# Performance work log

Measured on AMD Instinct MI355X. Metric: run time of the kernel, lower is better.

The kernel has to match this reference:

```python
import jax, jax.numpy as jnp
import numpy as np

K_MASK = -2.3819763e+38
NUM_HEADS = 16
NUM_KV_HEADS = 8
FEATURES = 2048
HEAD_DIM = 128
WINDOW = 1024
SOFT_CAP = 50.0
B, T = 2, 2048


def apply_rope(inputs, positions, head_dim, max_wavelength=10000):
    # inputs: [B, T, N, H], positions: [B, T]
    fraction = 2 * jnp.arange(0, head_dim // 2) / head_dim
    timescale = max_wavelength ** fraction
    sinusoid_inp = positions[..., None] / timescale[None, None, :]  # [B,T,H/2]
    sinusoid_inp = sinusoid_inp[..., None, :]  # [B,T,1,H/2]
    sin = jnp.sin(sinusoid_inp)
    cos = jnp.cos(sinusoid_inp)
    first_half, second_half = jnp.split(inputs, 2, axis=-1)
    first_part = first_half * cos - second_half * sin
    second_part = second_half * cos + first_half * sin
    return jnp.concatenate([first_part, second_part], axis=-1).astype(inputs.dtype)


def setup_inputs() -> dict:
    key = jax.random.key(0)
    k1, k2, k3, k4 = jax.random.split(key, 4)
    std = 0.02
    x = jax.random.normal(k1, (B, T, FEATURES), dtype=jnp.float32)
    segment_pos = jnp.broadcast_to(jnp.arange(T, dtype=jnp.int32), (B, T))
    # causal prefill mask [B, T, T]
    attn_mask = jnp.broadcast_to(jnp.tril(jnp.ones((T, T), dtype=bool)), (B, T, T))
    wq = jax.random.normal(k2, (NUM_HEADS, FEATURES, HEAD_DIM), dtype=jnp.float32) * std
    wkv = jax.random.normal(k3, (2, NUM_KV_HEADS, FEATURES, HEAD_DIM), dtype=jnp.float32) * std
    wo = jax.random.normal(k4, (NUM_HEADS, HEAD_DIM, FEATURES), dtype=jnp.float32) * std
    return {"x": x, "segment_pos": segment_pos, "attn_mask": attn_mask,
            "wq": wq, "wkv": wkv, "wo": wo}


def reference(x, segment_pos, attn_mask, wq, wkv, wo):
    # Projections (GQA path: num_kv_heads != num_heads)
    q = jnp.einsum('BTD,NDH->BTNH', x, wq)              # [B,T,N,H]
    k = jnp.einsum('BSD,KDH->BSKH', x, wkv[0])          # [B,S,K,H]
    v = jnp.einsum('BSD,KDH->BSKH', x, wkv[1])          # [B,S,K,H]

    q = apply_rope(q, segment_pos, HEAD_DIM)
    q = q * HEAD_DIM ** (-0.5)
    k = apply_rope(k, segment_pos, HEAD_DIM)

    b, t, n, h = q.shape
    g = n // NUM_KV_HEADS
    qg = q.reshape(b, t, NUM_KV_HEADS, g, h)
    logits = jnp.einsum('BTKGH,BSKH->BTKGS', qg, k)
    s = logits.shape[-1]
    logits = logits.reshape(b, t, n, s)

    # soft cap
    logits = jnp.tanh(logits / SOFT_CAP) * SOFT_CAP

    # sliding-window mask combined with attn_mask
    cache_positions = jnp.arange(s)[None, None, :]
    sp = segment_pos[:, :, None]
    sliding_mask = (cache_positions >= sp - WINDOW + 1) & (cache_positions <= sp + WINDOW - 1)
    mask = sliding_mask & attn_mask  # [B,T,S]

    padded_logits = jnp.where(mask[:, :, None, :], logits, K_MASK)
    probs = jax.nn.softmax(padded_logits, axis=-1).astype(k.dtype)

    pg = probs.reshape(b, t, NUM_KV_HEADS, g, s)
    encoded = jnp.einsum('BTKGS,BSKH->BTKGH', pg, v).reshape(b, t, n, h)
    attn_output = jnp.einsum('BTNH,NHD->BTD', encoded, wo)
    return attn_output
```

## Files before the change

### kernel.cpp

```cpp
#include <hip/hip_runtime.h>

typedef unsigned short u16;
typedef unsigned int u32;
typedef __attribute__((ext_vector_type(8))) short bfx8;
typedef __attribute__((ext_vector_type(4))) float fx4;

static __device__ __forceinline__ float b2f(u16 u) {
    union { float f; u32 i; } c; c.i = ((u32)u) << 16; return c.f;
}
static __device__ __forceinline__ u16 f2b(float f) {
    union { float f; u32 i; } c; c.f = f;
    u32 r = c.i + 0x7FFFu + ((c.i >> 16) & 1u);
    return (u16)(r >> 16);
}
typedef const __attribute__((address_space(1))) unsigned int* gas1;
typedef __attribute__((address_space(3))) unsigned int* las3;
static __device__ __forceinline__ void gll16(const void* g, void* l) {
    __builtin_amdgcn_global_load_lds((gas1)g, (las3)l, 16, 0, 0);
}

__global__ __launch_bounds__(256) void k_convert_x(const float* __restrict__ x, u16* __restrict__ xb) {
    size_t i = ((size_t)blockIdx.x * 256 + threadIdx.x) * 8;
    float4 a = *(const float4*)(x + i);
    float4 b = *(const float4*)(x + i + 4);
    union { u16 e[8]; uint4 v; } o;
    o.e[0] = f2b(a.x); o.e[1] = f2b(a.y); o.e[2] = f2b(a.z); o.e[3] = f2b(a.w);
    o.e[4] = f2b(b.x); o.e[5] = f2b(b.y); o.e[6] = f2b(b.z); o.e[7] = f2b(b.w);
    *(uint4*)(xb + i) = o.v;
}

__global__ __launch_bounds__(256) void k_pack_w1(const float* __restrict__ wq, const float* __restrict__ wkv,
                                                 u16* __restrict__ wb1) {
    __shared__ float t[128 * 33];
    int ci = blockIdx.x;
    int k0 = blockIdx.y << 5;
    int c0 = ci << 7;
    const float* src;
    if (ci < 16)      src = wq  + (size_t)ci * 2048 * 128;
    else if (ci < 24) src = wkv + (size_t)(ci - 16) * 2048 * 128;
    else              src = wkv + (size_t)(8 + ci - 24) * 2048 * 128;
    int tid = threadIdx.x;
#pragma unroll
    for (int i = 0; i < 16; i++) {
        int idx = i * 256 + tid;
        int kk = idx >> 7, cc = idx & 127;
        t[cc * 33 + kk] = src[(size_t)(k0 + kk) * 128 + cc];
    }
    __syncthreads();
#pragma unroll
    for (int i = 0; i < 16; i++) {
        int idx = i * 256 + tid;
        int cc = idx >> 5, kk = idx & 31;
        wb1[(size_t)(c0 + cc) * 2048 + k0 + kk] = f2b(t[cc * 33 + kk]);
    }
}

__global__ __launch_bounds__(256) void k_pack_w2(const float* __restrict__ wo, u16* __restrict__ wb2) {
    __shared__ float t[128 * 33];
    int c0 = blockIdx.x << 7;
    int k0 = blockIdx.y << 5;
    int tid = threadIdx.x;
#pragma unroll
    for (int i = 0; i < 16; i++) {
        int idx = i * 256 + tid;
        int kk = idx >> 7, cc = idx & 127;
        t[cc * 33 + kk] = wo[(size_t)(k0 + kk) * 2048 + c0 + cc];
    }
    __syncthreads();
#pragma unroll
    for (int i = 0; i < 16; i++) {
        int idx = i * 256 + tid;
        int cc = idx >> 5, kk = idx & 31;
        wb2[(size_t)(c0 + cc) * 2048 + k0 + kk] = f2b(t[cc * 33 + kk]);
    }
}

template <int BM, int OUT_BF16>
__global__ __launch_bounds__(512, 2) void k_gemm256(const u16* __restrict__ A, const u16* __restrict__ Bt,
                                                    void* __restrict__ C, int M, int N, int K) {
    constexpr int MF = BM / 32;
    constexpr int NA = BM / 16;
    constexpr int FR = NA + 16;
    constexpr int LPW = FR / 8;
    __shared__ u16 lds[4 * FR * 512];

    int tid = threadIdx.x, wave = tid >> 6, lane = tid & 63;
    int quad = lane >> 4, l16 = lane & 15;
    int wm = wave >> 2, wn = wave & 3;

    int nwg = gridDim.x * gridDim.y;
    int bid = blockIdx.y * gridDim.x + blockIdx.x;
    int swz = (bid & 7) * (nwg >> 3) + (bid >> 3);
    int bx = swz % gridDim.x, by = swz / gridDim.x;
    int r0 = by * BM, c0 = bx << 8;

    fx4 zero = {0.f, 0.f, 0.f, 0.f};
    fx4 acc[MF][4];
#pragma unroll
    for (int m = 0; m < MF; m++)
#pragma unroll
        for (int n = 0; n < 4; n++) acc[m][n] = zero;

    const u16* gsrc[LPW];
#pragma unroll
    for (int j = 0; j < LPW; j++) {
        int fw = wave * LPW + j;
        gsrc[j] = (fw < NA ? A + (size_t)(r0 + fw * 16 + l16) * K
                           : Bt + (size_t)(c0 + (fw - NA) * 16 + l16) * K) + quad * 8;
    }
    u16* ldst = lds + wave * (LPW * 512);

    int NT = K >> 5;
#pragma unroll
    for (int p = 0; p < 3; p++)
#pragma unroll
        for (int j = 0; j < LPW; j++) gll16(gsrc[j] + p * 32, ldst + p * (FR * 512) + j * 512);

    asm volatile("s_waitcnt vmcnt(%0)" : : "n"(2 * LPW) : "memory");
    __builtin_amdgcn_s_barrier();

    bfx8 cbf[4], caf[4];
#pragma unroll
    for (int n = 0; n < 4; n++) cbf[n] = *(const bfx8*)(lds + (NA + wn * 4 + n) * 512 + lane * 8);
#pragma unroll
    for (int m = 0; m < 4; m++) caf[m] = *(const bfx8*)(lds + (wm * MF + m) * 512 + lane * 8);

    for (int t = 0; t < NT; ++t) {
        const u16* Fb = lds + (t & 3) * (FR * 512);
        bfx8 nbf[4], naf[4], af1[4];
        bool has_next = (t + 1 < NT);
        if (has_next) {
            if (t + 2 < NT) asm volatile("s_waitcnt vmcnt(%0)" : : "n"(LPW) : "memory");
            else            asm volatile("s_waitcnt vmcnt(0)" : : : "memory");
            __builtin_amdgcn_s_barrier();
            if (t + 3 < NT) {
                u16* dst = lds + ((t + 3) & 3) * (FR * 512) + wave * (LPW * 512);
#pragma unroll
                for (int j = 0; j < LPW; j++) gll16(gsrc[j] + (size_t)(t + 3) * 32, dst + j * 512);
            }
        }
        if constexpr (MF == 8) {
#pragma unroll
            for (int m = 0; m < 4; m++) af1[m] = *(const bfx8*)(Fb + (wm * MF + 4 + m) * 512 + lane * 8);
        }
        if (has_next) {
            const u16* Fn = lds + ((t + 1) & 3) * (FR * 512);
#pragma unroll
            for (int n = 0; n < 4; n++) nbf[n] = *(const bfx8*)(Fn + (NA + wn * 4 + n) * 512 + lane * 8);
#pragma unroll
            for (int m = 0; m < 4; m++) naf[m] = *(const bfx8*)(Fn + (wm * MF + m) * 512 + lane * 8);
        }
        __builtin_amdgcn_s_setprio(1);
#pragma unroll
        for (int m = 0; m < 4; m++)
#pragma unroll
            for (int n = 0; n < 4; n++)
                acc[m][n] = __builtin_amdgcn_mfma_f32_16x16x32_bf16(caf[m], cbf[n], acc[m][n], 0, 0, 0);
        __builtin_amdgcn_s_setprio(0);
        if constexpr (MF == 8) {
            __builtin_amdgcn_s_setprio(1);
#pragma unroll
            for (int m = 0; m < 4; m++)
#pragma unroll
                for (int n = 0; n < 4; n++)
                    acc[4 + m][n] = __builtin_amdgcn_mfma_f32_16x16x32_bf16(af1[m], cbf[n], acc[4 + m][n], 0, 0, 0);
            __builtin_amdgcn_s_setprio(0);
        }
        if (has_next) {
#pragma unroll
            for (int n = 0; n < 4; n++) cbf[n] = nbf[n];
#pragma unroll
            for (int m = 0; m < 4; m++) caf[m] = naf[m];
        }
    }
#pragma unroll
    for (int m = 0; m < MF; m++)
#pragma unroll
        for (int n = 0; n < 4; n++) {
            int col = c0 + wn * 64 + n * 16 + l16;
#pragma unroll
            for (int r = 0; r < 4; r++) {
                int row = r0 + wm * (BM / 2) + m * 16 + quad * 4 + r;
                float v = acc[m][n][r];
                if (OUT_BF16) ((u16*)C)[(size_t)row * N + col] = f2b(v);
                else          ((float*)C)[(size_t)row * N + col] = v;
            }
        }
}

__global__ __launch_bounds__(256) void k_rope(const u16* __restrict__ qkv, u16* __restrict__ Qb,
                                              u16* __restrict__ Kb, u16* __restrict__ Vb) {
    __shared__ float sc[128];
    int bt = blockIdx.x;
    int b = bt >> 11, t = bt & 2047;
    const u16* row = qkv + (size_t)bt * 4096;
    int tid = threadIdx.x;
    float tf = (float)t;
    const float RS = 0.08838834764831845f;
    const float LT = 0.20762050593046f;
    if (tid < 64) {
        float ang = tf * exp2f(-LT * (float)tid);
        float s, c; sincosf(ang, &s, &c);
        sc[tid] = s; sc[tid + 64] = c;
    }
    __syncthreads();
#pragma unroll
    for (int i = 0; i < 4; i++) {
        int idx = tid + i * 256;
        int n = idx >> 6, hp = idx & 63;
        float x1 = b2f(row[n * 128 + hp]);
        float x2 = b2f(row[n * 128 + hp + 64]);
        float s = sc[hp], c = sc[hp + 64];
        size_t o = ((size_t)(b * 16 + n) * 2048 + t) * 128 + hp;
        Qb[o]      = f2b((x1 * c - x2 * s) * RS);
        Qb[o + 64] = f2b((x2 * c + x1 * s) * RS);
    }
#pragma unroll
    for (int i = 0; i < 2; i++) {
        int idx = tid + i * 256;
        int kh = idx >> 6, hp = idx & 63;
        float x1 = b2f(row[2048 + kh * 128 + hp]);
        float x2 = b2f(row[2048 + kh * 128 + hp + 64]);
        float s = sc[hp], c = sc[hp + 64];
        size_t o = ((size_t)(b * 8 + kh) * 2048 + t) * 128 + hp;
        Kb[o]      = f2b(x1 * c - x2 * s);
        Kb[o + 64] = f2b(x2 * c + x1 * s);
    }
#pragma unroll
    for (int i = 0; i < 4; i++) {
        int idx = tid + i * 256;
        int kh = idx >> 7, h = idx & 127;
        Vb[((size_t)(b * 8 + kh) * 2048 + t) * 128 + h] = row[3072 + idx];
    }
}

__global__ __launch_bounds__(256) void k_transpose_v(const u16* __restrict__ Vb, u16* __restrict__ Vt) {
    __shared__ u16 t[128 * 136];
    int bk = blockIdx.y;
    int t0 = blockIdx.x << 7;
    const u16* src = Vb + ((size_t)bk * 2048 + t0) * 128;
    u16* dst = Vt + (size_t)bk * 128 * 2048 + t0;
    int tid = threadIdx.x;
#pragma unroll
    for (int it = 0; it < 8; it++) {
        int ch = tid + it * 256;
        int tt = ch >> 4, c8 = (ch & 15) << 3;
        *(uint4*)(t + tt * 136 + c8) = *(const uint4*)(src + (size_t)tt * 128 + c8);
    }
    __syncthreads();
#pragma unroll
    for (int it = 0; it < 8; it++) {
        int ch = tid + it * 256;
        int h = ch >> 4, s8 = (ch & 15) << 3;
        union { uint4 v; u16 e[8]; } vv;
#pragma unroll
        for (int j = 0; j < 8; j++) vv.e[j] = t[(s8 + j) * 136 + h];
        *(uint4*)(dst + (size_t)h * 2048 + s8) = vv.v;
    }
}

__global__ __launch_bounds__(512, 4) void k_attn(const u16* __restrict__ Qb, const u16* __restrict__ Kb,
                                                 const u16* __restrict__ Vt, u16* __restrict__ enc) {
    __shared__ u16 Ks[2][16 * 512];
    __shared__ u16 Vs[2][16 * 512];
    __shared__ u16 Pl[8 * 1024];
    int t0 = blockIdx.x << 6;
    int kh = blockIdx.y, b = blockIdx.z;
    int tid = threadIdx.x, wave = tid >> 6, lane = tid & 63;
    int quad = lane >> 4, l16 = lane & 15;
    int n = (kh << 1) + (wave >> 2);
    int tw = t0 + ((wave & 3) << 4);
    const u16* Qp = Qb + (size_t)(b * 16 + n) * 2048 * 128;
    const u16* Kp = Kb + (size_t)(b * 8 + kh) * 2048 * 128;
    const u16* Vp = Vt + (size_t)(b * 8 + kh) * 128 * 2048;

    bfx8 aq[4];
#pragma unroll
    for (int kb = 0; kb < 4; kb++)
        aq[kb] = *(const bfx8*)(Qp + (size_t)(tw + l16) * 128 + kb * 32 + quad * 8);

    const u16* kgp[2]; const u16* vgp[2];
#pragma unroll
    for (int q = 0; q < 2; q++) {
        int f = wave * 2 + q;
        kgp[q] = Kp + (size_t)((f >> 2) * 16 + l16) * 128 + (f & 3) * 32 + quad * 8;
        vgp[q] = Vp + (size_t)((f >> 1) * 16 + l16) * 2048 + (f & 1) * 32 + quad * 8;
    }
    u16* Pw = Pl + wave * 1024;

    fx4 zero = {0.f, 0.f, 0.f, 0.f};
    fx4 o_acc[8];
#pragma unroll
    for (int hb = 0; hb < 8; hb++) o_acc[hb] = zero;
    float lsum[4] = {0.f, 0.f, 0.f, 0.f};

    const float C1 = 0.057707801635559f;
    const float C2 = 144.269504088896f;

    int s_lo = t0 - 1023; if (s_lo < 0) s_lo = 0;
    int ts0 = s_lo >> 6, ts1 = t0 >> 6;

#pragma unroll
    for (int q = 0; q < 2; q++) {
        int f = wave * 2 + q;
        gll16(kgp[q] + (size_t)(ts0 << 6) * 128, Ks[0] + f * 512);
        gll16(vgp[q] + (ts0 << 6), Vs[0] + f * 512);
    }

    for (int ts = ts0; ts <= ts1; ts++) {
        int cur = (ts - ts0) & 1;
        int s0 = ts << 6;
        __builtin_amdgcn_s_barrier();
        if (ts < ts1) {
            int s1 = (ts + 1) << 6;
#pragma unroll
            for (int q = 0; q < 2; q++) {
                int f = wave * 2 + q;
                gll16(kgp[q] + (size_t)s1 * 128, Ks[cur ^ 1] + f * 512);
                gll16(vgp[q] + s1, Vs[cur ^ 1] + f * 512);
            }
            asm volatile("s_waitcnt vmcnt(4)" : : : "memory");
        } else {
            asm volatile("s_waitcnt vmcnt(0)" : : : "memory");
        }
        __builtin_amdgcn_s_barrier();

        if (s0 <= tw + 15 && s0 + 63 >= tw - 1023) {
            const u16* Kc = Ks[cur];
            const u16* Vc = Vs[cur];
            bool full = (s0 + 63 <= tw) && (s0 >= tw - 1008);
            if (full) {
#pragma unroll
                for (int nb = 0; nb < 4; nb++) {
                    fx4 sacc = zero;
                    __builtin_amdgcn_s_setprio(1);
#pragma unroll
                    for (int kb = 0; kb < 4; kb++) {
                        bfx8 bk = *(const bfx8*)(Kc + (nb * 4 + kb) * 512 + lane * 8);
                        sacc = __builtin_amdgcn_mfma_f32_16x16x32_bf16(aq[kb], bk, sacc, 0, 0, 0);
                    }
                    __builtin_amdgcn_s_setprio(0);
                    int base0 = ((nb >> 1) * 64 + ((nb & 1) * 2 + (l16 >> 3)) * 16 + quad * 4) * 8 + (l16 & 7);
#pragma unroll
                    for (int r = 0; r < 4; r++) {
                        float u = __builtin_amdgcn_exp2f(sacc[r] * C1);
                        float p = __builtin_amdgcn_exp2f(-C2 * __builtin_amdgcn_rcpf(u + 1.f));
                        lsum[r] += p;
                        Pw[base0 + r * 8] = f2b(p);
                    }
                }
            } else {
#pragma unroll
                for (int nb = 0; nb < 4; nb++) {
                    int sb = s0 + (nb << 4);
                    int base0 = ((nb >> 1) * 64 + ((nb & 1) * 2 + (l16 >> 3)) * 16 + quad * 4) * 8 + (l16 & 7);
                    if (sb <= tw + 15 && sb + 15 >= tw - 1023) {
                        fx4 sacc = zero;
#pragma unroll
                        for (int kb = 0; kb < 4; kb++) {
                            bfx8 bk = *(const bfx8*)(Kc + (nb * 4 + kb) * 512 + lane * 8);
                            sacc = __builtin_amdgcn_mfma_f32_16x16x32_bf16(aq[kb], bk, sacc, 0, 0, 0);
                        }
                        int sg = sb + l16;
#pragma unroll
                        for (int r = 0; r < 4; r++) {
                            int tg = tw + quad * 4 + r;
                            float u = __builtin_amdgcn_exp2f(sacc[r] * C1);
                            float p = __builtin_amdgcn_exp2f(-C2 * __builtin_amdgcn_rcpf(u + 1.f));
                            p = (sg <= tg && sg >= tg - 1023) ? p : 0.f;
                            lsum[r] += p;
                            Pw[base0 + r * 8] = f2b(p);
                        }
                    } else {
#pragma unroll
                        for (int r = 0; r < 4; r++) Pw[base0 + r * 8] = 0;
                    }
                }
            }
            asm volatile("s_waitcnt lgkmcnt(0)" : : : "memory");
            __builtin_amdgcn_sched_barrier(0);
            bfx8 pf[2];
#pragma unroll
            for (int kk = 0; kk < 2; kk++)
                pf[kk] = *(const bfx8*)(Pw + kk * 512 + lane * 8);
            __builtin_amdgcn_s_setprio(1);
#pragma unroll
            for (int hb = 0; hb < 8; hb++)
#pragma unroll
                for (int kk = 0; kk < 2; kk++) {
                    bfx8 vf = *(const bfx8*)(Vc + (hb * 2 + kk) * 512 + lane * 8);
                    o_acc[hb] = __builtin_amdgcn_mfma_f32_16x16x32_bf16(pf[kk], vf, o_acc[hb], 0, 0, 0);
                }
            __builtin_amdgcn_s_setprio(0);
        }
    }
#pragma unroll
    for (int r = 0; r < 4; r++) {
#pragma unroll
        for (int off = 1; off < 16; off <<= 1)
            lsum[r] += __shfl_xor(lsum[r], off);
        lsum[r] = 1.0f / lsum[r];
    }
#pragma unroll
    for (int hb = 0; hb < 8; hb++) {
        int h = hb * 16 + l16;
#pragma unroll
        for (int r = 0; r < 4; r++) {
            int tg = tw + quad * 4 + r;
            enc[((size_t)(b * 2048 + tg) * 16 + n) * 128 + h] = f2b(o_acc[hb][r] * lsum[r]);
        }
    }
}

extern "C" void kernel_launch(void* const* d_in, const int* in_sizes, int n_in,
                              void* d_out, int out_size, void* d_ws, size_t ws_size,
                              hipStream_t stream) {
    const float* x   = (const float*)d_in[0];
    const float* wq  = (const float*)d_in[3];
    const float* wkv = (const float*)d_in[4];
    const float* wo  = (const float*)d_in[5];
    char* ws = (char*)d_ws;
    const size_t MiB = 1024 * 1024;
    u16* xb  = (u16*)(ws);
    u16* wb1 = (u16*)(ws + 16 * MiB);
    u16* qkv = (u16*)(ws + 32 * MiB);
    u16* Qb  = (u16*)(ws);
    u16* Kb  = (u16*)(ws + 16 * MiB);
    u16* Vb  = (u16*)(ws + 24 * MiB);
    u16* enc = (u16*)(ws + 32 * MiB);
    u16* wb2 = (u16*)(ws + 48 * MiB);
    u16* Vt  = (u16*)(ws + 56 * MiB);

    k_convert_x<<<4096, 256, 0, stream>>>(x, xb);
    k_pack_w1<<<dim3(32, 64), 256, 0, stream>>>(wq, wkv, wb1);
    k_gemm256<256, 1><<<dim3(16, 16), 512, 0, stream>>>(xb, wb1, qkv, 4096, 4096, 2048);
    k_rope<<<4096, 256, 0, stream>>>(qkv, Qb, Kb, Vb);
    k_transpose_v<<<dim3(16, 16), 256, 0, stream>>>(Vb, Vt);
    k_pack_w2<<<dim3(16, 64), 256, 0, stream>>>(wo, wb2);
    k_attn<<<dim3(32, 8, 2), 512, 0, stream>>>(Qb, Kb, Vt, enc);
    k_gemm256<128, 0><<<dim3(8, 32), 512, 0, stream>>>(enc, wb2, d_out, 4096, 2048, 2048);
}
```

Baseline: 352.1 us.

## Merge prep kernels and split GEMM main loop into interleaved half-steps

Combines x conversion with wq/wkv packing, and V transpose with wo packing, into two merged kernels, cutting the launch count from 8 to 6. The GEMM main loop is unrolled by two with register double-buffering (aA/bA, aB/bB). Each K-step is split into two MFMA halves, with the global-to-LDS prefetch issued in two parts around an extra barrier. The aim is to overlap loads with MFMA work and remove the register copy of the next fragments, at the cost of an extra barrier per step and more register pressure.

```diff
diff --git a/kernel.cpp b/kernel.cpp
--- a/kernel.cpp
+++ b/kernel.cpp
@@ -19,69 +19,100 @@
     __builtin_amdgcn_global_load_lds((gas1)g, (las3)l, 16, 0, 0);
 }
 
-__global__ __launch_bounds__(256) void k_convert_x(const float* __restrict__ x, u16* __restrict__ xb) {
-    size_t i = ((size_t)blockIdx.x * 256 + threadIdx.x) * 8;
-    float4 a = *(const float4*)(x + i);
-    float4 b = *(const float4*)(x + i + 4);
-    union { u16 e[8]; uint4 v; } o;
-    o.e[0] = f2b(a.x); o.e[1] = f2b(a.y); o.e[2] = f2b(a.z); o.e[3] = f2b(a.w);
-    o.e[4] = f2b(b.x); o.e[5] = f2b(b.y); o.e[6] = f2b(b.z); o.e[7] = f2b(b.w);
-    *(uint4*)(xb + i) = o.v;
-}
-
-__global__ __launch_bounds__(256) void k_pack_w1(const float* __restrict__ wq, const float* __restrict__ wkv,
-                                                 u16* __restrict__ wb1) {
+__global__ __launch_bounds__(256) void k_prep1(const float* __restrict__ x, u16* __restrict__ xb,
+                                               const float* __restrict__ wq, const float* __restrict__ wkv,
+                                               u16* __restrict__ wb1) {
     __shared__ float t[128 * 33];
-    int ci = blockIdx.x;
-    int k0 = blockIdx.y << 5;
+    int bid = blockIdx.x, tid = threadIdx.x;
+    if (bid < 4096) {
+        size_t i = ((size_t)bid * 256 + tid) * 8;
+        float4 a = *(const float4*)(x + i);
+        float4 b = *(const float4*)(x + i + 4);
+        union { u16 e[8]; uint4 v; } o;
+        o.e[0] = f2b(a.x); o.e[1] = f2b(a.y); o.e[2] = f2b(a.z); o.e[3] = f2b(a.w);
+        o.e[4] = f2b(b.x); o.e[5] = f2b(b.y); o.e[6] = f2b(b.z); o.e[7] = f2b(b.w);
+        *(uint4*)(xb + i) = o.v;
+        return;
+    }
+    int idx = bid - 4096;
+    int ci = idx & 31;
+    int k0 = (idx >> 5) << 5;
     int c0 = ci << 7;
     const float* src;
     if (ci < 16)      src = wq  + (size_t)ci * 2048 * 128;
     else if (ci < 24) src = wkv + (size_t)(ci - 16) * 2048 * 128;
     else              src = wkv + (size_t)(8 + ci - 24) * 2048 * 128;
-    int tid = threadIdx.x;
 #pragma unroll
     for (int i = 0; i < 16; i++) {
-        int idx = i * 256 + tid;
-        int kk = idx >> 7, cc = idx & 127;
+        int id2 = i * 256 + tid;
+        int kk = id2 >> 7, cc = id2 & 127;
         t[cc * 33 + kk] = src[(size_t)(k0 + kk) * 128 + cc];
     }
     __syncthreads();
 #pragma unroll
     for (int i = 0; i < 16; i++) {
-        int idx = i * 256 + tid;
-        int cc = idx >> 5, kk = idx & 31;
+        int id2 = i * 256 + tid;
+        int cc = id2 >> 5, kk = id2 & 31;
         wb1[(size_t)(c0 + cc) * 2048 + k0 + kk] = f2b(t[cc * 33 + kk]);
     }
 }
 
-__global__ __launch_bounds__(256) void k_pack_w2(const float* __restrict__ wo, u16* __restrict__ wb2) {
-    __shared__ float t[128 * 33];
-    int c0 = blockIdx.x << 7;
-    int k0 = blockIdx.y << 5;
-    int tid = threadIdx.x;
+__global__ __launch_bounds__(256) void k_prep2(const u16* __restrict__ Vb, u16* __restrict__ Vt,
+                                               const float* __restrict__ wo, u16* __restrict__ wb2) {
+    __shared__ __align__(16) char smem[128 * 136 * 2];
+    int bid = blockIdx.x, tid = threadIdx.x;
+    if (bid < 256) {
+        u16* t = (u16*)smem;
+        int bk = bid >> 4;
+        int t0 = (bid & 15) << 7;
+        const u16* src = Vb + ((size_t)bk * 2048 + t0) * 128;
+        u16* dst = Vt + (size_t)bk * 128 * 2048 + t0;
+#pragma unroll
+        for (int it = 0; it < 8; it++) {
+            int ch = tid + it * 256;
+            int tt = ch >> 4, c8 = (ch & 15) << 3;
+            *(uint4*)(t + tt * 136 + c8) = *(const uint4*)(src + (size_t)tt * 128 + c8);
+        }
+        __syncthreads();
+#pragma unroll
+        for (int it = 0; it < 8; it++) {
+            int ch = tid + it * 256;
+            int h = ch >> 4, s8 = (ch & 15) << 3;
+            union { uint4 v; u16 e[8]; } vv;
+#pragma unroll
+            for (int j = 0; j < 8; j++) vv.e[j] = t[(s8 + j) * 136 + h];
+            *(uint4*)(dst + (size_t)h * 2048 + s8) = vv.v;
+        }
+        return;
+    }
+    float* t = (float*)smem;
+    int idx = bid - 256;
+    int c0 = (idx & 15) << 7;
+    int k0 = (idx >> 4) << 5;
 #pragma unroll
     for (int i = 0; i < 16; i++) {
-        int idx = i * 256 + tid;
-        int kk = idx >> 7, cc = idx & 127;
+        int id2 = i * 256 + tid;
+        int kk = id2 >> 7, cc = id2 & 127;
         t[cc * 33 + kk] = wo[(size_t)(k0 + kk) * 2048 + c0 + cc];
     }
     __syncthreads();
 #pragma unroll
     for (int i = 0; i < 16; i++) {
-        int idx = i * 256 + tid;
-        int cc = idx >> 5, kk = idx & 31;
+        int id2 = i * 256 + tid;
+        int cc = id2 >> 5, kk = id2 & 31;
         wb2[(size_t)(c0 + cc) * 2048 + k0 + kk] = f2b(t[cc * 33 + kk]);
     }
 }
 
 template <int BM, int OUT_BF16>
-__global__ __launch_bounds__(512, 2) void k_gemm256(const u16* __restrict__ A, const u16* __restrict__ Bt,
-                                                    void* __restrict__ C, int M, int N, int K) {
+__global__ __launch_bounds__(512, 2) void k_gemm16(const u16* __restrict__ A, const u16* __restrict__ Bt,
+                                                   void* __restrict__ C, int M, int N, int K) {
     constexpr int MF = BM / 32;
     constexpr int NA = BM / 16;
     constexpr int FR = NA + 16;
     constexpr int LPW = FR / 8;
+    constexpr int S1 = 2;
+    constexpr int S2 = LPW - 2;
     __shared__ u16 lds[4 * FR * 512];
 
     int tid = threadIdx.x, wave = tid >> 6, lane = tid & 63;
@@ -119,60 +150,120 @@
     asm volatile("s_waitcnt vmcnt(%0)" : : "n"(2 * LPW) : "memory");
     __builtin_amdgcn_s_barrier();
 
-    bfx8 cbf[4], caf[4];
-#pragma unroll
-    for (int n = 0; n < 4; n++) cbf[n] = *(const bfx8*)(lds + (NA + wn * 4 + n) * 512 + lane * 8);
-#pragma unroll
-    for (int m = 0; m < 4; m++) caf[m] = *(const bfx8*)(lds + (wm * MF + m) * 512 + lane * 8);
-
-    for (int t = 0; t < NT; ++t) {
-        const u16* Fb = lds + (t & 3) * (FR * 512);
-        bfx8 nbf[4], naf[4], af1[4];
-        bool has_next = (t + 1 < NT);
-        if (has_next) {
-            if (t + 2 < NT) asm volatile("s_waitcnt vmcnt(%0)" : : "n"(LPW) : "memory");
-            else            asm volatile("s_waitcnt vmcnt(0)" : : : "memory");
+    bfx8 aA[4], bA[4], aB[4], bB[4], af1[4];
+#pragma unroll
+    for (int n = 0; n < 4; n++) bA[n] = *(const bfx8*)(lds + (NA + wn * 4 + n) * 512 + lane * 8);
+#pragma unroll
+    for (int m = 0; m < 4; m++) aA[m] = *(const bfx8*)(lds + (wm * MF + m) * 512 + lane * 8);
+
+#define STG(tt, j0, cnt) { u16* dst = lds + ((tt) & 3) * (FR * 512) + wave * (LPW * 512);                  \
+    _Pragma("unroll") for (int j = 0; j < (cnt); j++)                                                      \
+        gll16(gsrc[(j0) + j] + (size_t)(tt) * 32, dst + ((j0) + j) * 512); }
+
+    for (int t = 0; t < NT; t += 2) {
+        if (t + 2 < NT) asm volatile("s_waitcnt vmcnt(%0)" : : "n"(LPW) : "memory");
+        else            asm volatile("s_waitcnt vmcnt(0)" : : : "memory");
+        __builtin_amdgcn_s_barrier();
+        {
+            const u16* Fb = lds + (t & 3) * (FR * 512);
+            const u16* Fn = lds + ((t + 1) & 3) * (FR * 512);
+            if (t + 3 < NT) STG(t + 3, 0, S1);
+            if constexpr (MF == 8) {
+#pragma unroll
+                for (int m = 0; m < 4; m++) af1[m] = *(const bfx8*)(Fb + (wm * MF + 4 + m) * 512 + lane * 8);
+            }
+#pragma unroll
+            for (int n = 0; n < 4; n++) bB[n] = *(const bfx8*)(Fn + (NA + wn * 4 + n) * 512 + lane * 8);
+            __builtin_amdgcn_s_setprio(1);
+            if constexpr (MF == 8) {
+#pragma unroll
+                for (int m = 0; m < 4; m++)
+#pragma unroll
+                    for (int n = 0; n < 4; n++)
+                        acc[m][n] = __builtin_amdgcn_mfma_f32_16x16x32_bf16(aA[m], bA[n], acc[m][n], 0, 0, 0);
+            } else {
+#pragma unroll
+                for (int m = 0; m < 2; m++)
+#pragma unroll
+                    for (int n = 0; n < 4; n++)
+                        acc[m][n] = __builtin_amdgcn_mfma_f32_16x16x32_bf16(aA[m], bA[n], acc[m][n], 0, 0, 0);
+            }
+            __builtin_amdgcn_s_setprio(0);
             __builtin_amdgcn_s_barrier();
-            if (t + 3 < NT) {
-                u16* dst = lds + ((t + 3) & 3) * (FR * 512) + wave * (LPW * 512);
-#pragma unroll
-                for (int j = 0; j < LPW; j++) gll16(gsrc[j] + (size_t)(t + 3) * 32, dst + j * 512);
-            }
-        }
-        if constexpr (MF == 8) {
-#pragma unroll
-            for (int m = 0; m < 4; m++) af1[m] = *(const bfx8*)(Fb + (wm * MF + 4 + m) * 512 + lane * 8);
-        }
-        if (has_next) {
-            const u16* Fn = lds + ((t + 1) & 3) * (FR * 512);
-#pragma unroll
-            for (int n = 0; n < 4; n++) nbf[n] = *(const bfx8*)(Fn + (NA + wn * 4 + n) * 512 + lane * 8);
-#pragma unroll
-            for (int m = 0; m < 4; m++) naf[m] = *(const bfx8*)(Fn + (wm * MF + m) * 512 + lane * 8);
-        }
-        __builtin_amdgcn_s_setprio(1);
-#pragma unroll
-        for (int m = 0; m < 4; m++)
-#pragma unroll
-            for (int n = 0; n < 4; n++)
-                acc[m][n] = __builtin_amdgcn_mfma_f32_16x16x32_bf16(caf[m], cbf[n], acc[m][n], 0, 0, 0);
-        __builtin_amdgcn_s_setprio(0);
-        if constexpr (MF == 8) {
+            if (t + 3 < NT) STG(t + 3, S1, S2);
+#pragma unroll
+            for (int m = 0; m < 4; m++) aB[m] = *(const bfx8*)(Fn + (wm * MF + m) * 512 + lane * 8);
             __builtin_amdgcn_s_setprio(1);
-#pragma unroll
-            for (int m = 0; m < 4; m++)
-#pragma unroll
-                for (int n = 0; n < 4; n++)
-                    acc[4 + m][n] = __builtin_amdgcn_mfma_f32_16x16x32_bf16(af1[m], cbf[n], acc[4 + m][n], 0, 0, 0);
+            if constexpr (MF == 8) {
+#pragma unroll
+                for (int m = 0; m < 4; m++)
+#pragma unroll
+                    for (int n = 0; n < 4; n++)
+                        acc[4 + m][n] = __builtin_amdgcn_mfma_f32_16x16x32_bf16(af1[m], bA[n], acc[4 + m][n], 0, 0, 0);
+            } else {
+#pragma unroll
+                for (int m = 2; m < 4; m++)
+#pragma unroll
+                    for (int n = 0; n < 4; n++)
+                        acc[m][n] = __builtin_amdgcn_mfma_f32_16x16x32_bf16(aA[m], bA[n], acc[m][n], 0, 0, 0);
+            }
             __builtin_amdgcn_s_setprio(0);
         }
-        if (has_next) {
-#pragma unroll
-            for (int n = 0; n < 4; n++) cbf[n] = nbf[n];
-#pragma unroll
-            for (int m = 0; m < 4; m++) caf[m] = naf[m];
-        }
-    }
+        if (t + 3 < NT) asm volatile("s_waitcnt vmcnt(%0)" : : "n"(LPW) : "memory");
+        else            asm volatile("s_waitcnt vmcnt(0)" : : : "memory");
+        __builtin_amdgcn_s_barrier();
+        {
+            const u16* Fb = lds + ((t + 1) & 3) * (FR * 512);
+            const u16* Fn = lds + ((t + 2) & 3) * (FR * 512);
+            bool hn = (t + 2 < NT);
+            if (t + 4 < NT) STG(t + 4, 0, S1);
+            if constexpr (MF == 8) {
+#pragma unroll
+                for (int m = 0; m < 4; m++) af1[m] = *(const bfx8*)(Fb + (wm * MF + 4 + m) * 512 + lane * 8);
+            }
+            if (hn) {
+#pragma unroll
+                for (int n = 0; n < 4; n++) bA[n] = *(const bfx8*)(Fn + (NA + wn * 4 + n) * 512 + lane * 8);
+            }
+            __builtin_amdgcn_s_setprio(1);
+            if constexpr (MF == 8) {
+#pragma unroll
+                for (int m = 0; m < 4; m++)
+#pragma unroll
+                    for (int n = 0; n < 4; n++)
+                        acc[m][n] = __builtin_amdgcn_mfma_f32_16x16x32_bf16(aB[m], bB[n], acc[m][n], 0, 0, 0);
+            } else {
+#pragma unroll
+                for (int m = 0; m < 2; m++)
+#pragma unroll
+                    for (int n = 0; n < 4; n++)
+                        acc[m][n] = __builtin_amdgcn_mfma_f32_16x16x32_bf16(aB[m], bB[n], acc[m][n], 0, 0, 0);
+            }
+            __builtin_amdgcn_s_setprio(0);
+            __builtin_amdgcn_s_barrier();
+            if (t + 4 < NT) STG(t + 4, S1, S2);
+            if (hn) {
+#pragma unroll
+                for (int m = 0; m < 4; m++) aA[m] = *(const bfx8*)(Fn + (wm * MF + m) * 512 + lane * 8);
+            }
+            __builtin_amdgcn_s_setprio(1);
+            if constexpr (MF == 8) {
+#pragma unroll
+                for (int m = 0; m < 4; m++)
+#pragma unroll
+                    for (int n = 0; n < 4; n++)
+                        acc[4 + m][n] = __builtin_amdgcn_mfma_f32_16x16x32_bf16(af1[m], bB[n], acc[4 + m][n], 0, 0, 0);
+            } else {
+#pragma unroll
+                for (int m = 2; m < 4; m++)
+#pragma unroll
+                    for (int n = 0; n < 4; n++)
+                        acc[m][n] = __builtin_amdgcn_mfma_f32_16x16x32_bf16(aB[m], bB[n], acc[m][n], 0, 0, 0);
+            }
+            __builtin_amdgcn_s_setprio(0);
+        }
+    }
+#undef STG
 #pragma unroll
     for (int m = 0; m < MF; m++)
 #pragma unroll
@@ -231,31 +322,6 @@
         int idx = tid + i * 256;
         int kh = idx >> 7, h = idx & 127;
         Vb[((size_t)(b * 8 + kh) * 2048 + t) * 128 + h] = row[3072 + idx];
-    }
-}
-
-__global__ __launch_bounds__(256) void k_transpose_v(const u16* __restrict__ Vb, u16* __restrict__ Vt) {
-    __shared__ u16 t[128 * 136];
-    int bk = blockIdx.y;
-    int t0 = blockIdx.x << 7;
-    const u16* src = Vb + ((size_t)bk * 2048 + t0) * 128;
-    u16* dst = Vt + (size_t)bk * 128 * 2048 + t0;
-    int tid = threadIdx.x;
-#pragma unroll
-    for (int it = 0; it < 8; it++) {
-        int ch = tid + it * 256;
-        int tt = ch >> 4, c8 = (ch & 15) << 3;
-        *(uint4*)(t + tt * 136 + c8) = *(const uint4*)(src + (size_t)tt * 128 + c8);
-    }
-    __syncthreads();
-#pragma unroll
-    for (int it = 0; it < 8; it++) {
-        int ch = tid + it * 256;
-        int h = ch >> 4, s8 = (ch & 15) << 3;
-        union { uint4 v; u16 e[8]; } vv;
-#pragma unroll
-        for (int j = 0; j < 8; j++) vv.e[j] = t[(s8 + j) * 136 + h];
-        *(uint4*)(dst + (size_t)h * 2048 + s8) = vv.v;
     }
 }
 
@@ -431,12 +497,10 @@
     u16* wb2 = (u16*)(ws + 48 * MiB);
     u16* Vt  = (u16*)(ws + 56 * MiB);
 
-    k_convert_x<<<4096, 256, 0, stream>>>(x, xb);
-    k_pack_w1<<<dim3(32, 64), 256, 0, stream>>>(wq, wkv, wb1);
-    k_gemm256<256, 1><<<dim3(16, 16), 512, 0, stream>>>(xb, wb1, qkv, 4096, 4096, 2048);
+    k_prep1<<<6144, 256, 0, stream>>>(x, xb, wq, wkv, wb1);
+    k_gemm16<256, 1><<<dim3(16, 16), 512, 0, stream>>>(xb, wb1, qkv, 4096, 4096, 2048);
     k_rope<<<4096, 256, 0, stream>>>(qkv, Qb, Kb, Vb);
-    k_transpose_v<<<dim3(16, 16), 256, 0, stream>>>(Vb, Vt);
-    k_pack_w2<<<dim3(16, 64), 256, 0, stream>>>(wo, wb2);
+    k_prep2<<<1280, 256, 0, stream>>>(Vb, Vt, wo, wb2);
     k_attn<<<dim3(32, 8, 2), 512, 0, stream>>>(Qb, Kb, Vt, enc);
-    k_gemm256<128, 0><<<dim3(8, 32), 512, 0, stream>>>(enc, wb2, d_out, 4096, 2048, 2048);
-}
+    k_gemm16<128, 0><<<dim3(8, 32), 512, 0, stream>>>(enc, wb2, d_out, 4096, 2048, 2048);
+}
```

Result: faster. 341.8 us (-2.9%).
